# Kernel optimization log

Hardware: AMD Instinct MI355X
Metric: run time of the kernel (lower is better)

The kernel has to match this reference:

```python
import jax, jax.numpy as jnp
import numpy as np

S, B, IN, H, DFF, OUT, L, NHEAD, WINDOW = 2048, 4, 64, 1024, 1024, 64, 3, 4, 4
EPS = 1e-5


def _layer_norm(x, scale, bias):
    m = jnp.mean(x, axis=-1, keepdims=True)
    v = jnp.var(x, axis=-1, keepdims=True)
    return (x - m) * jax.lax.rsqrt(v + EPS) * scale + bias


def setup_inputs() -> dict:
    key = jax.random.key(0)
    ks = jax.random.split(key, 12)
    s = 0.02
    return {
        "src": jax.random.normal(ks[0], (S, B, IN), dtype=jnp.float32),
        "Wenc": jax.random.normal(ks[1], (H, IN), dtype=jnp.float32) * s,
        "benc": jnp.zeros((H,), jnp.float32),
        "Wqkv": jax.random.normal(ks[2], (L, 3 * H, H), dtype=jnp.float32) * s,
        "bqkv": jnp.zeros((L, 3 * H), jnp.float32),
        "Wo": jax.random.normal(ks[3], (L, H, H), dtype=jnp.float32) * s,
        "bo": jnp.zeros((L, H), jnp.float32),
        "W1": jax.random.normal(ks[4], (L, DFF, H), dtype=jnp.float32) * s,
        "b1": jnp.zeros((L, DFF), jnp.float32),
        "W2": jax.random.normal(ks[5], (L, H, DFF), dtype=jnp.float32) * s,
        "b2": jnp.zeros((L, H), jnp.float32),
        "ln1_s": jnp.ones((L, H), jnp.float32),
        "ln1_b": jnp.zeros((L, H), jnp.float32),
        "ln2_s": jnp.ones((L, H), jnp.float32),
        "ln2_b": jnp.zeros((L, H), jnp.float32),
        "Wout": jax.random.normal(ks[6], (OUT, H), dtype=jnp.float32) * s,
        "bout": jnp.zeros((OUT,), jnp.float32),
    }


def _banded_mask(sz):
    # triu(1) masked + lower-band (j < i-4) masked => allowed: i-4 <= j <= i
    i = jnp.arange(sz)[:, None]
    j = jnp.arange(sz)[None, :]
    allowed = (j <= i) & (j >= i - WINDOW)
    return jnp.where(allowed, 0.0, -1e9).astype(jnp.float32)


def reference(src, Wenc, benc, Wqkv, bqkv, Wo, bo, W1, b1, W2, b2,
              ln1_s, ln1_b, ln2_s, ln2_b, Wout, bout):
    dh = H // NHEAD
    mask = _banded_mask(src.shape[0])  # [S, S]
    x = src @ Wenc.T + benc  # [S, B, H]  (NOTE: pos_encoder is never applied in the source)

    def layer(x, p):
        Wqkv_, bqkv_, Wo_, bo_, W1_, b1_, W2_, b2_, s1, g1, s2, g2 = p
        qkv = x @ Wqkv_.T + bqkv_  # [S, B, 3H]
        q, k, v = jnp.split(qkv, 3, axis=-1)
        sS, sB = x.shape[0], x.shape[1]
        q = q.reshape(sS, sB, NHEAD, dh)
        k = k.reshape(sS, sB, NHEAD, dh)
        v = v.reshape(sS, sB, NHEAD, dh)
        scores = jnp.einsum('sbhd,tbhd->bhst', q, k) / jnp.sqrt(jnp.float32(dh))
        scores = scores + mask  # broadcast over [b, h]
        attn = jax.nn.softmax(scores, axis=-1)
        ctx = jnp.einsum('bhst,tbhd->sbhd', attn, v).reshape(sS, sB, H)
        attn_out = ctx @ Wo_.T + bo_
        x = _layer_norm(x + attn_out, s1, g1)  # post-norm (PyTorch default)
        ff = jax.nn.relu(x @ W1_.T + b1_) @ W2_.T + b2_
        x = _layer_norm(x + ff, s2, g2)
        return x, None

    x, _ = jax.lax.scan(layer, x, (Wqkv, bqkv, Wo, bo, W1, b1, W2, b2,
                                   ln1_s, ln1_b, ln2_s, ln2_b))
    return x @ Wout.T + bout  # [S, B, OUT]
```

## Files before the change

### kernel.cpp

```cpp
#include <hip/hip_runtime.h>
#include <hip/hip_bf16.h>

#define S_LEN   2048
#define BATCH   4
#define IN_DIM  64
#define H_DIM   1024
#define DFF_DIM 1024
#define OUT_DIM 64
#define NLAYER  3
#define NHEADS  4
#define DHEAD   256
#define WIN     4
#define ROWS    (S_LEN*BATCH)
#define QKV_LD  (3*H_DIM)


typedef __bf16 bf16x8 __attribute__((ext_vector_type(8)));
typedef float  f32x4  __attribute__((ext_vector_type(4)));

__device__ __forceinline__ float bfbits2f(unsigned int u) {
  union { unsigned int i; float f; } c; c.i = u << 16; return c.f;
}
__device__ __forceinline__ unsigned short f2bfbits(float f) {
  __hip_bfloat16 h = __float2bfloat16(f);
  return __builtin_bit_cast(unsigned short, h);
}

__device__ __forceinline__ void g2l16(const void* g, void* l) {
  __builtin_amdgcn_global_load_lds((__attribute__((address_space(1))) void*)g,
                                   (__attribute__((address_space(3))) void*)l,
                                   16, 0, 0);
}

struct CvtSeg { const float* src; __hip_bfloat16* dst; int n4; };

__global__ __launch_bounds__(256)
void cvt_all_k(CvtSeg s0, CvtSeg s1, CvtSeg s2, CvtSeg s3,
               CvtSeg s4, CvtSeg s5, CvtSeg s6)
{
  int i = blockIdx.x * 256 + threadIdx.x;
  CvtSeg seg;
  if      (i < s0.n4) { seg = s0; }
  else if ((i -= s0.n4) < s1.n4) { seg = s1; }
  else if ((i -= s1.n4) < s2.n4) { seg = s2; }
  else if ((i -= s2.n4) < s3.n4) { seg = s3; }
  else if ((i -= s3.n4) < s4.n4) { seg = s4; }
  else if ((i -= s4.n4) < s5.n4) { seg = s5; }
  else if ((i -= s5.n4) < s6.n4) { seg = s6; }
  else return;
  float4 v = *(const float4*)(seg.src + (size_t)i * 4);
  uint2 o;
  o.x = (unsigned)f2bfbits(v.x) | ((unsigned)f2bfbits(v.y) << 16);
  o.y = (unsigned)f2bfbits(v.z) | ((unsigned)f2bfbits(v.w) << 16);
  *(uint2*)(seg.dst + (size_t)i * 4) = o;
}

template<int RELU, int OUTF32, int ADDRES>
__global__ __launch_bounds__(256, 2)
void gemm_bt(const __hip_bfloat16* __restrict__ A, int lda,
             const __hip_bfloat16* __restrict__ B,
             const float* __restrict__ bias,
             void* __restrict__ Cp, int ldc,
             const __hip_bfloat16* __restrict__ R, int ldr,
             int M, int N, int K)
{
  __shared__ __align__(16) __hip_bfloat16 As[128 * 64];
  __shared__ __align__(16) __hip_bfloat16 Bs[128 * 64];

  const int tid  = threadIdx.x;
  const int lane = tid & 63;
  const int wave = tid >> 6;
  const int quad = lane >> 4;
  const int l16  = lane & 15;

  const int gx  = gridDim.x;
  const int lin = blockIdx.y * gx + blockIdx.x;
  const int gsz = 4 * gx;
  const int mt  = (lin / gsz) * 4 + (lin & 3);
  const int nt  = (lin % gsz) >> 2;
  const int m0 = mt * 128;
  const int n0 = nt * 128;

  const int wr = (wave >> 1) * 64;
  const int wc = (wave & 1) * 64;

  int arow[4], acol[4], brow[4];
#pragma unroll
  for (int s = 0; s < 4; s++) {
    const int p = tid + (s << 8);
    arow[s] = p >> 3;
    acol[s] = ((p & 7) ^ ((p >> 3) & 7)) * 8;
    brow[s] = min(n0 + arow[s], N - 1);
  }

  f32x4 acc[4][4] = {};
  const int nk = K >> 6;

  for (int t = 0; t < nk; ++t) {
    const int k0 = t << 6;
#pragma unroll
    for (int s = 0; s < 4; s++) {
      const int lo = (wave * 64 + (s << 8)) * 8;
      g2l16(A + (size_t)(m0 + arow[s]) * lda + k0 + acol[s], &As[lo]);
      g2l16(B + (size_t)brow[s] * K + k0 + acol[s], &Bs[lo]);
    }
    __syncthreads();

#pragma unroll
    for (int kh = 0; kh < 2; kh++) {
      bf16x8 af[4], bfr[4];
#pragma unroll
      for (int i = 0; i < 4; i++) {
        const int row = wr + i * 16 + l16;
        const int c   = (kh * 4 + quad) ^ (row & 7);
        af[i] = *(const bf16x8*)&As[row * 64 + c * 8];
      }
#pragma unroll
      for (int j = 0; j < 4; j++) {
        const int row = wc + j * 16 + l16;
        const int c   = (kh * 4 + quad) ^ (row & 7);
        bfr[j] = *(const bf16x8*)&Bs[row * 64 + c * 8];
      }
#pragma unroll
      for (int i = 0; i < 4; i++)
#pragma unroll
        for (int j = 0; j < 4; j++)
          acc[i][j] = __builtin_amdgcn_mfma_f32_16x16x32_bf16(af[i], bfr[j], acc[i][j], 0, 0, 0);
    }
    __syncthreads();
  }

#pragma unroll
  for (int j = 0; j < 4; j++) {
    int col = n0 + wc + j * 16 + l16;
    if (col < N) {
      float bv = bias[col];
#pragma unroll
      for (int i = 0; i < 4; i++) {
        int row = m0 + wr + i * 16 + quad * 4;
#pragma unroll
        for (int r = 0; r < 4; r++) {
          float v = acc[i][j][r] + bv;
          if (RELU) v = fmaxf(v, 0.f);
          if (ADDRES) v += __bfloat162float(R[(size_t)(row + r) * ldr + col]);
          if (OUTF32) ((float*)Cp)[(size_t)(row + r) * ldc + col] = v;
          else ((__hip_bfloat16*)Cp)[(size_t)(row + r) * ldc + col] = __float2bfloat16(v);
        }
      }
    }
  }
}

__global__ __launch_bounds__(256)
void attn_k(__hip_bfloat16* __restrict__ qkv)
{
  const int gw   = (blockIdx.x << 2) + (threadIdx.x >> 6);
  const int lane = threadIdx.x & 63;
  const int h = gw & (NHEADS - 1);
  const int b = (gw >> 2) & (BATCH - 1);
  const int s = gw >> 4;
  const size_t hoff = (size_t)h * DHEAD + (lane << 2);

  float q0, q1, q2, q3;
  {
    uint2 t = *(const uint2*)(qkv + (size_t)(s * BATCH + b) * QKV_LD + hoff);
    q0 = bfbits2f(t.x & 0xffff); q1 = bfbits2f(t.x >> 16);
    q2 = bfbits2f(t.y & 0xffff); q3 = bfbits2f(t.y >> 16);
  }

  float sc[WIN + 1];
#pragma unroll
  for (int jj = 0; jj <= WIN; jj++) {
    int j = s - WIN + jj;
    float v = -1e30f;
    if (j >= 0) {
      uint2 t = *(const uint2*)(qkv + (size_t)(j * BATCH + b) * QKV_LD + H_DIM + hoff);
      float p = q0 * bfbits2f(t.x & 0xffff) + q1 * bfbits2f(t.x >> 16)
              + q2 * bfbits2f(t.y & 0xffff) + q3 * bfbits2f(t.y >> 16);
#pragma unroll
      for (int o = 32; o; o >>= 1) p += __shfl_xor(p, o);
      v = p * 0.0625f;
    }
    sc[jj] = v;
  }

  float mx = sc[0];
#pragma unroll
  for (int jj = 1; jj <= WIN; jj++) mx = fmaxf(mx, sc[jj]);
  float p[WIN + 1], den = 0.f;
#pragma unroll
  for (int jj = 0; jj <= WIN; jj++) { p[jj] = __expf(sc[jj] - mx); den += p[jj]; }

  float a0 = 0.f, a1 = 0.f, a2 = 0.f, a3 = 0.f;
#pragma unroll
  for (int jj = 0; jj <= WIN; jj++) {
    int j = s - WIN + jj;
    if (j >= 0) {
      uint2 t = *(const uint2*)(qkv + (size_t)(j * BATCH + b) * QKV_LD + 2 * H_DIM + hoff);
      a0 += p[jj] * bfbits2f(t.x & 0xffff); a1 += p[jj] * bfbits2f(t.x >> 16);
      a2 += p[jj] * bfbits2f(t.y & 0xffff); a3 += p[jj] * bfbits2f(t.y >> 16);
    }
  }
  float rl = 1.f / den;
  uint2 o;
  o.x = (unsigned)f2bfbits(a0 * rl) | ((unsigned)f2bfbits(a1 * rl) << 16);
  o.y = (unsigned)f2bfbits(a2 * rl) | ((unsigned)f2bfbits(a3 * rl) << 16);
  *(uint2*)(qkv + (size_t)(s * BATCH + b) * QKV_LD + hoff) = o;
}

__global__ __launch_bounds__(256)
void ln_k(const __hip_bfloat16* __restrict__ y, int ys,
          const float* __restrict__ g, const float* __restrict__ be,
          __hip_bfloat16* __restrict__ xout)
{
  const int row  = blockIdx.x * 4 + (threadIdx.x >> 6);
  const int lane = threadIdx.x & 63;
  const int e0   = lane * 16;
  const __hip_bfloat16* yp = y + (size_t)row * ys + e0;

  uint2 v[4];
  *(uint4*)&v[0] = *(const uint4*)yp;
  *(uint4*)&v[2] = *(const uint4*)(yp + 8);
  float t[16];
#pragma unroll
  for (int k = 0; k < 4; k++) {
    t[k * 4 + 0] = bfbits2f(v[k].x & 0xffff);
    t[k * 4 + 1] = bfbits2f(v[k].x >> 16);
    t[k * 4 + 2] = bfbits2f(v[k].y & 0xffff);
    t[k * 4 + 3] = bfbits2f(v[k].y >> 16);
  }
  float s = 0.f, ss = 0.f;
#pragma unroll
  for (int k = 0; k < 16; k++) { s += t[k]; ss += t[k] * t[k]; }
#pragma unroll
  for (int o = 32; o; o >>= 1) { s += __shfl_xor(s, o); ss += __shfl_xor(ss, o); }

  const float inv  = 1.f / (float)H_DIM;
  const float mean = s * inv;
  const float var  = ss * inv - mean * mean;
  const float rstd = rsqrtf(var + 1e-5f);

  float4 gv[4], bv[4];
#pragma unroll
  for (int k = 0; k < 4; k++) {
    gv[k] = *(const float4*)(g + e0 + k * 4);
    bv[k] = *(const float4*)(be + e0 + k * 4);
  }
  uint2 ob[4];
#pragma unroll
  for (int k = 0; k < 4; k++) {
    float o0 = (t[k*4+0] - mean) * rstd * gv[k].x + bv[k].x;
    float o1 = (t[k*4+1] - mean) * rstd * gv[k].y + bv[k].y;
    float o2 = (t[k*4+2] - mean) * rstd * gv[k].z + bv[k].z;
    float o3 = (t[k*4+3] - mean) * rstd * gv[k].w + bv[k].w;
    ob[k].x = (unsigned)f2bfbits(o0) | ((unsigned)f2bfbits(o1) << 16);
    ob[k].y = (unsigned)f2bfbits(o2) | ((unsigned)f2bfbits(o3) << 16);
  }
  __hip_bfloat16* xp = xout + (size_t)row * H_DIM + e0;
  *(uint4*)xp       = *(const uint4*)&ob[0];
  *(uint4*)(xp + 8) = *(const uint4*)&ob[2];
}

extern "C" void kernel_launch(void* const* d_in, const int* in_sizes, int n_in,
                              void* d_out, int out_size, void* d_ws, size_t ws_size,
                              hipStream_t stream) {
  const float* src   = (const float*)d_in[0];
  const float* Wenc  = (const float*)d_in[1];
  const float* benc  = (const float*)d_in[2];
  const float* Wqkv  = (const float*)d_in[3];
  const float* bqkv  = (const float*)d_in[4];
  const float* Wo    = (const float*)d_in[5];
  const float* bo    = (const float*)d_in[6];
  const float* W1    = (const float*)d_in[7];
  const float* b1    = (const float*)d_in[8];
  const float* W2    = (const float*)d_in[9];
  const float* b2    = (const float*)d_in[10];
  const float* ln1s  = (const float*)d_in[11];
  const float* ln1b  = (const float*)d_in[12];
  const float* ln2s  = (const float*)d_in[13];
  const float* ln2b  = (const float*)d_in[14];
  const float* Wout  = (const float*)d_in[15];
  const float* bout  = (const float*)d_in[16];

  char* ws = (char*)d_ws;
  __hip_bfloat16* WB   = (__hip_bfloat16*)ws;
  __hip_bfloat16* srcb = WB;
  __hip_bfloat16* wenc = WB + 524288;
  __hip_bfloat16* wqkv = WB + 589824;
  __hip_bfloat16* wo   = WB + 10027008;
  __hip_bfloat16* w1   = WB + 13172736;
  __hip_bfloat16* w2   = WB + 16318464;
  __hip_bfloat16* wout = WB + 19464192;
  __hip_bfloat16* xb  = (__hip_bfloat16*)(ws + (size_t)40 * 1048576);
  __hip_bfloat16* qkv = (__hip_bfloat16*)(ws + (size_t)56 * 1048576);
  __hip_bfloat16* ctxp = qkv;
  __hip_bfloat16* ybuf = qkv + H_DIM;
  __hip_bfloat16* hbuf = qkv + 2 * H_DIM;

  const dim3 blk(256);

  {
    CvtSeg s0{src,  srcb, 524288 / 4};
    CvtSeg s1{Wenc, wenc, 65536 / 4};
    CvtSeg s2{Wqkv, wqkv, 9437184 / 4};
    CvtSeg s3{Wo,   wo,   3145728 / 4};
    CvtSeg s4{W1,   w1,   3145728 / 4};
    CvtSeg s5{W2,   w2,   3145728 / 4};
    CvtSeg s6{Wout, wout, 65536 / 4};
    const int tot4 = (524288 + 65536 + 9437184 + 3 * 3145728 + 65536) / 4;
    cvt_all_k<<<dim3((tot4 + 255) / 256), blk, 0, stream>>>(s0, s1, s2, s3, s4, s5, s6);
  }

  gemm_bt<0, 0, 0><<<dim3(H_DIM / 128, ROWS / 128), blk, 0, stream>>>(
      srcb, IN_DIM, wenc, benc, xb, H_DIM, nullptr, 0, ROWS, H_DIM, IN_DIM);

  for (int l = 0; l < NLAYER; l++) {
    gemm_bt<0, 0, 0><<<dim3(QKV_LD / 128, ROWS / 128), blk, 0, stream>>>(
        xb, H_DIM, wqkv + (size_t)l * QKV_LD * H_DIM, bqkv + l * QKV_LD,
        qkv, QKV_LD, nullptr, 0, ROWS, QKV_LD, H_DIM);
    attn_k<<<dim3(ROWS * NHEADS / 4), blk, 0, stream>>>(qkv);
    gemm_bt<0, 0, 1><<<dim3(H_DIM / 128, ROWS / 128), blk, 0, stream>>>(
        ctxp, QKV_LD, wo + (size_t)l * H_DIM * H_DIM, bo + l * H_DIM,
        ybuf, QKV_LD, xb, H_DIM, ROWS, H_DIM, H_DIM);
    ln_k<<<dim3(ROWS / 4), blk, 0, stream>>>(ybuf, QKV_LD, ln1s + l * H_DIM, ln1b + l * H_DIM, xb);
    gemm_bt<1, 0, 0><<<dim3(DFF_DIM / 128, ROWS / 128), blk, 0, stream>>>(
        xb, H_DIM, w1 + (size_t)l * DFF_DIM * H_DIM, b1 + l * DFF_DIM,
        hbuf, QKV_LD, nullptr, 0, ROWS, DFF_DIM, H_DIM);
    gemm_bt<0, 0, 1><<<dim3(H_DIM / 128, ROWS / 128), blk, 0, stream>>>(
        hbuf, QKV_LD, w2 + (size_t)l * H_DIM * DFF_DIM, b2 + l * H_DIM,
        ybuf, QKV_LD, xb, H_DIM, ROWS, H_DIM, DFF_DIM);
    ln_k<<<dim3(ROWS / 4), blk, 0, stream>>>(ybuf, QKV_LD, ln2s + l * H_DIM, ln2b + l * H_DIM, xb);
  }

  gemm_bt<0, 1, 0><<<dim3(1, ROWS / 128), blk, 0, stream>>>(
      xb, H_DIM, wout, bout, d_out, OUT_DIM, nullptr, 0, ROWS, OUT_DIM, H_DIM);
}
```

Before: 733.4 us.

## Add 256x256 8-wave pipelined GEMM kernel for QKV projection

Adds a new bf16 MFMA GEMM kernel with 512 threads, 256x256 output tiles, a double-buffered and XOR-swizzled LDS layout, and an 8-phase schedule that interleaves global-to-LDS prefetch with MFMA work. It also remaps blocks in groups of four M-tiles for L2 reuse. Only the QKV projection GEMM, the largest one per layer, uses it. The aim is more data reuse per tile and better overlap of memory traffic with compute. The cost is much higher register and LDS pressure, and the kernel assumes K is a multiple of 128 and dimensions divide exactly.

Measured after the change: 746.9 us. Within noise of the previous version (+1.8%).

```diff
diff --git a/kernel.cpp b/kernel.cpp
--- a/kernel.cpp
+++ b/kernel.cpp
@@ -149,6 +149,144 @@
       }
     }
   }
+}
+
+#define G8_STAGE(SLOTPTR, GBASE, LD)                                          \
+  do {                                                                        \
+    const __hip_bfloat16* gb_ = (GBASE);                                      \
+    g2l16(gb_ + (size_t)sr0 * (LD) + sc8x8, (SLOTPTR) + (wave << 9));         \
+    g2l16(gb_ + (size_t)sr1 * (LD) + sc8x8, (SLOTPTR) + 4096 + (wave << 9));  \
+  } while (0)
+
+#define G8_PHASE(BUF, QM, QN, STAGE_STMT, WAIT_STMT)                          \
+  do {                                                                        \
+    bf16x8 af[4][2], bfr[2][2];                                               \
+    const __hip_bfloat16* Asl = &lds[BUF][QM][0];                             \
+    const __hip_bfloat16* Bsl = &lds[BUF][2 + (QN)][0];                       \
+    _Pragma("unroll") for (int im = 0; im < 4; im++) {                        \
+      const int r = wrA + im * 16;                                            \
+      const int sw = r & 7;                                                   \
+      _Pragma("unroll") for (int ks = 0; ks < 2; ks++)                        \
+        af[im][ks] = *(const bf16x8*)&Asl[r * 64 + (((ks * 4 + quad) ^ sw) << 3)]; \
+    }                                                                         \
+    _Pragma("unroll") for (int jn = 0; jn < 2; jn++) {                        \
+      const int r = wrB + jn * 16;                                            \
+      const int sw = r & 7;                                                   \
+      _Pragma("unroll") for (int ks = 0; ks < 2; ks++)                        \
+        bfr[jn][ks] = *(const bf16x8*)&Bsl[r * 64 + (((ks * 4 + quad) ^ sw) << 3)]; \
+    }                                                                         \
+    STAGE_STMT;                                                               \
+    WAIT_STMT;                                                                \
+    __builtin_amdgcn_s_barrier();                                             \
+    asm volatile("s_waitcnt lgkmcnt(0)" ::: "memory");                        \
+    __builtin_amdgcn_sched_barrier(0);                                        \
+    __builtin_amdgcn_s_setprio(1);                                            \
+    _Pragma("unroll") for (int ks = 0; ks < 2; ks++)                          \
+      _Pragma("unroll") for (int im = 0; im < 4; im++)                        \
+        _Pragma("unroll") for (int jn = 0; jn < 2; jn++)                      \
+          acc[(QM) * 4 + im][(QN) * 2 + jn] =                                 \
+              __builtin_amdgcn_mfma_f32_16x16x32_bf16(                        \
+                  af[im][ks], bfr[jn][ks],                                    \
+                  acc[(QM) * 4 + im][(QN) * 2 + jn], 0, 0, 0);                \
+    __builtin_amdgcn_s_setprio(0);                                            \
+    __builtin_amdgcn_s_barrier();                                             \
+  } while (0)
+
+template<int RELU, int ADDRES>
+__global__ __launch_bounds__(512, 2)
+void gemm8_bt(const __hip_bfloat16* __restrict__ A, int lda,
+              const __hip_bfloat16* __restrict__ B,
+              const float* __restrict__ bias,
+              __hip_bfloat16* __restrict__ C, int ldc,
+              const __hip_bfloat16* __restrict__ Rr, int ldr,
+              int N, int K)
+{
+  __shared__ __align__(16) __hip_bfloat16 lds[2][4][128 * 64];
+
+  const int tid  = threadIdx.x;
+  const int lane = tid & 63;
+  const int wave = tid >> 6;
+  const int quad = lane >> 4;
+  const int l16  = lane & 15;
+  const int wm   = wave >> 2;
+  const int wn   = wave & 3;
+  const int wrA  = wm * 64 + l16;
+  const int wrB  = wn * 32 + l16;
+
+  const int sr0   = tid >> 3;
+  const int sr1   = sr0 + 64;
+  const int sc8x8 = (((tid & 7) ^ (sr0 & 7)) << 3);
+
+  const int gx  = gridDim.x;
+  const int lin = blockIdx.y * gx + blockIdx.x;
+  const int gsz = 4 * gx;
+  const int mt  = (lin / gsz) * 4 + (lin & 3);
+  const int nt  = (lin % gsz) >> 2;
+  const int m0 = mt * 256;
+  const int n0 = nt * 256;
+
+  const __hip_bfloat16* Ab = A + (size_t)m0 * lda;
+  const __hip_bfloat16* Bb = B + (size_t)n0 * K;
+
+  f32x4 acc[8][4] = {};
+  const int NI = K >> 7;
+
+  G8_STAGE(&lds[0][0][0], Ab, lda);
+  G8_STAGE(&lds[0][2][0], Bb, K);
+  G8_STAGE(&lds[0][1][0], Ab + (size_t)128 * lda, lda);
+  G8_STAGE(&lds[0][3][0], Bb + (size_t)128 * K, K);
+  G8_STAGE(&lds[1][0][0], Ab + 64, lda);
+  G8_STAGE(&lds[1][2][0], Bb + 64, K);
+  asm volatile("s_waitcnt vmcnt(4)" ::: "memory");
+  __builtin_amdgcn_s_barrier();
+
+  for (int i = 0; i < NI; ++i) {
+    const int k1 = (2 * i + 1) << 6;
+    const int k2 = k1 + 64;
+    const int k3 = k1 + 128;
+    const bool pf = (i + 1 < NI);
+
+    G8_PHASE(0, 0, 0,
+             G8_STAGE(&lds[1][1][0], Ab + (size_t)128 * lda + k1, lda), );
+    G8_PHASE(0, 0, 1,
+             G8_STAGE(&lds[1][3][0], Bb + (size_t)128 * K + k1, K), );
+    G8_PHASE(0, 1, 0,
+             if (pf) G8_STAGE(&lds[0][0][0], Ab + k2, lda), );
+    G8_PHASE(0, 1, 1,
+             if (pf) G8_STAGE(&lds[0][2][0], Bb + k2, K),
+             if (pf) { asm volatile("s_waitcnt vmcnt(4)" ::: "memory"); }
+             else    { asm volatile("s_waitcnt vmcnt(0)" ::: "memory"); });
+    G8_PHASE(1, 0, 0,
+             if (pf) G8_STAGE(&lds[0][1][0], Ab + (size_t)128 * lda + k2, lda), );
+    G8_PHASE(1, 0, 1,
+             if (pf) G8_STAGE(&lds[0][3][0], Bb + (size_t)128 * K + k2, K), );
+    G8_PHASE(1, 1, 0,
+             if (pf) G8_STAGE(&lds[1][0][0], Ab + k3, lda), );
+    G8_PHASE(1, 1, 1,
+             if (pf) G8_STAGE(&lds[1][2][0], Bb + k3, K),
+             asm volatile("s_waitcnt vmcnt(4)" ::: "memory"));
+  }
+
+#pragma unroll
+  for (int qm = 0; qm < 2; qm++)
+#pragma unroll
+    for (int im = 0; im < 4; im++)
+#pragma unroll
+      for (int qn = 0; qn < 2; qn++)
+#pragma unroll
+        for (int jn = 0; jn < 2; jn++) {
+          const int row0 = m0 + qm * 128 + wm * 64 + im * 16 + quad * 4;
+          const int col  = n0 + qn * 128 + wn * 32 + jn * 16 + l16;
+          const float bv = bias[col];
+          const f32x4 a  = acc[qm * 4 + im][qn * 2 + jn];
+#pragma unroll
+          for (int r = 0; r < 4; r++) {
+            float v = a[r] + bv;
+            if (RELU) v = fmaxf(v, 0.f);
+            if (ADDRES) v += __bfloat162float(Rr[(size_t)(row0 + r) * ldr + col]);
+            C[(size_t)(row0 + r) * ldc + col] = __float2bfloat16(v);
+          }
+        }
 }
 
 __global__ __launch_bounds__(256)
@@ -315,9 +453,9 @@
       srcb, IN_DIM, wenc, benc, xb, H_DIM, nullptr, 0, ROWS, H_DIM, IN_DIM);
 
   for (int l = 0; l < NLAYER; l++) {
-    gemm_bt<0, 0, 0><<<dim3(QKV_LD / 128, ROWS / 128), blk, 0, stream>>>(
+    gemm8_bt<0, 0><<<dim3(QKV_LD / 256, ROWS / 256), dim3(512), 0, stream>>>(
         xb, H_DIM, wqkv + (size_t)l * QKV_LD * H_DIM, bqkv + l * QKV_LD,
-        qkv, QKV_LD, nullptr, 0, ROWS, QKV_LD, H_DIM);
+        qkv, QKV_LD, nullptr, 0, QKV_LD, H_DIM);
     attn_k<<<dim3(ROWS * NHEADS / 4), blk, 0, stream>>>(qkv);
     gemm_bt<0, 0, 1><<<dim3(H_DIM / 128, ROWS / 128), blk, 0, stream>>>(
         ctxp, QKV_LD, wo + (size_t)l * H_DIM * H_DIM, bo + l * H_DIM,
```

## Add triple-buffered 128x256 GEMM kernel with async LDS loads for layer GEMMs

Applied to the files above, without the earlier changes.

Introduces a new 512-thread GEMM kernel that uses 128x256 tiles, a three-stage LDS ring buffer filled by direct global-to-LDS loads, XOR-swizzled LDS layout, grouped tile rasterization, and split-phase prefetch interleaved with MFMA issue under raised wave priority. All four per-layer GEMMs switch to it. The aim is to hide global memory latency behind matrix work and raise per-block reuse over the older 128x128 kernel. In exchange it uses much more LDS per block, limiting occupancy to one block per CU, and it relies on the dimensions being exact multiples of the tile sizes.

Result: faster. 697.7 us (-4.9%).

```diff
diff --git a/kernel.cpp b/kernel.cpp
--- a/kernel.cpp
+++ b/kernel.cpp
@@ -146,6 +146,134 @@
           if (OUTF32) ((float*)Cp)[(size_t)(row + r) * ldc + col] = v;
           else ((__hip_bfloat16*)Cp)[(size_t)(row + r) * ldc + col] = __float2bfloat16(v);
         }
+      }
+    }
+  }
+}
+
+#define R3_SA(BUF, KO)                                                        \
+  do {                                                                        \
+    __hip_bfloat16* d_ = &lds[BUF][0];                                        \
+    _Pragma("unroll") for (int s_ = 0; s_ < 2; s_++)                          \
+      g2l16(Ab + (size_t)arow[s_] * lda + (KO) + acol[s_],                    \
+            d_ + (((wave << 6) + (s_ << 9)) << 3));                           \
+  } while (0)
+#define R3_SB0(BUF, KO)                                                       \
+  do {                                                                        \
+    __hip_bfloat16* d_ = &lds[BUF][8192];                                     \
+    _Pragma("unroll") for (int s_ = 0; s_ < 2; s_++)                          \
+      g2l16(Bb + (size_t)arow[s_] * K + (KO) + acol[s_],                      \
+            d_ + (((wave << 6) + (s_ << 9)) << 3));                           \
+  } while (0)
+#define R3_SB1(BUF, KO)                                                       \
+  do {                                                                        \
+    __hip_bfloat16* d_ = &lds[BUF][8192];                                     \
+    _Pragma("unroll") for (int s_ = 2; s_ < 4; s_++)                          \
+      g2l16(Bb + (size_t)arow[s_] * K + (KO) + acol[s_],                      \
+            d_ + (((wave << 6) + (s_ << 9)) << 3));                           \
+  } while (0)
+
+#define R3_PH(BUF, KS, STAGE_STMT, WAIT_STMT)                                 \
+  do {                                                                        \
+    bf16x8 af[4], bq[4];                                                      \
+    const __hip_bfloat16* As_ = &lds[BUF][0];                                 \
+    const __hip_bfloat16* Bs_ = &lds[BUF][8192];                              \
+    _Pragma("unroll") for (int im = 0; im < 4; im++) {                        \
+      const int r_ = wm * 64 + im * 16 + l16;                                 \
+      af[im] = *(const bf16x8*)&As_[r_ * 64 + ((((KS)*4 + quad) ^ (r_ & 7)) << 3)]; \
+    }                                                                         \
+    _Pragma("unroll") for (int jn = 0; jn < 4; jn++) {                        \
+      const int r_ = wn * 64 + jn * 16 + l16;                                 \
+      bq[jn] = *(const bf16x8*)&Bs_[r_ * 64 + ((((KS)*4 + quad) ^ (r_ & 7)) << 3)]; \
+    }                                                                         \
+    STAGE_STMT;                                                               \
+    WAIT_STMT;                                                                \
+    __builtin_amdgcn_s_barrier();                                             \
+    asm volatile("s_waitcnt lgkmcnt(0)" ::: "memory");                        \
+    __builtin_amdgcn_sched_barrier(0);                                        \
+    __builtin_amdgcn_s_setprio(1);                                            \
+    _Pragma("unroll") for (int im = 0; im < 4; im++)                          \
+      _Pragma("unroll") for (int jn = 0; jn < 4; jn++)                        \
+        acc[im][jn] = __builtin_amdgcn_mfma_f32_16x16x32_bf16(                \
+            af[im], bq[jn], acc[im][jn], 0, 0, 0);                            \
+    __builtin_amdgcn_s_setprio(0);                                            \
+    __builtin_amdgcn_s_barrier();                                             \
+  } while (0)
+
+template<int RELU, int ADDRES>
+__global__ __launch_bounds__(512, 1)
+void gemm3r_bt(const __hip_bfloat16* __restrict__ A, int lda,
+               const __hip_bfloat16* __restrict__ B,
+               const float* __restrict__ bias,
+               __hip_bfloat16* __restrict__ C, int ldc,
+               const __hip_bfloat16* __restrict__ Rr, int ldr,
+               int K)
+{
+  __shared__ __align__(16) __hip_bfloat16 lds[3][24576];
+
+  const int tid  = threadIdx.x;
+  const int lane = tid & 63;
+  const int wave = tid >> 6;
+  const int quad = lane >> 4;
+  const int l16  = lane & 15;
+  const int wm   = wave >> 2;
+  const int wn   = wave & 3;
+
+  const int gx  = gridDim.x;
+  const int lin = blockIdx.y * gx + blockIdx.x;
+  const int gsz = 4 * gx;
+  const int mt  = (lin / gsz) * 4 + (lin & 3);
+  const int nt  = (lin % gsz) >> 2;
+  const int m0 = mt * 128;
+  const int n0 = nt * 256;
+
+  const __hip_bfloat16* Ab = A + (size_t)m0 * lda;
+  const __hip_bfloat16* Bb = B + (size_t)n0 * K;
+
+  int arow[4], acol[4];
+#pragma unroll
+  for (int s = 0; s < 4; s++) {
+    const int p = tid + (s << 9);
+    arow[s] = p >> 3;
+    acol[s] = ((p & 7) ^ (arow[s] & 7)) << 3;
+  }
+
+  f32x4 acc[4][4] = {};
+  const int NK = K >> 6;
+
+  R3_SA(0, 0);  R3_SB0(0, 0);  R3_SB1(0, 0);
+  R3_SA(1, 64); R3_SB0(1, 64); R3_SB1(1, 64);
+  asm volatile("s_waitcnt vmcnt(6)" ::: "memory");
+  __builtin_amdgcn_s_barrier();
+
+  for (int t = 0; t < NK; ++t) {
+    const int r  = t % 3;
+    const int rn = (t + 2) % 3;
+    const int k2 = (t + 2) << 6;
+    const bool pf = (t + 2) < NK;
+
+    R3_PH(r, 0,
+          if (pf) { R3_SA(rn, k2); R3_SB0(rn, k2); }, );
+    R3_PH(r, 1,
+          if (pf) { R3_SB1(rn, k2); },
+          if (pf) { asm volatile("s_waitcnt vmcnt(6)" ::: "memory"); }
+          else    { asm volatile("s_waitcnt vmcnt(0)" ::: "memory"); });
+  }
+
+#pragma unroll
+  for (int jn = 0; jn < 4; jn++) {
+    const int col = n0 + wn * 64 + jn * 16 + l16;
+    const float bv = bias[col];
+#pragma unroll
+    for (int im = 0; im < 4; im++) {
+      const int row0 = m0 + wm * 64 + im * 16 + quad * 4;
+      const f32x4 a = acc[im][jn];
+#pragma unroll
+      for (int rr = 0; rr < 4; rr++) {
+        float v = a[rr] + bv;
+        if (RELU) v = fmaxf(v, 0.f);
+        if (ADDRES) v += __bfloat162float(Rr[(size_t)(row0 + rr) * ldr + col]);
+        C[(size_t)(row0 + rr) * ldc + col] = __float2bfloat16(v);
       }
     }
   }
@@ -298,6 +426,7 @@
   __hip_bfloat16* hbuf = qkv + 2 * H_DIM;
 
   const dim3 blk(256);
+  const dim3 blk512(512);
 
   {
     CvtSeg s0{src,  srcb, 524288 / 4};
@@ -315,20 +444,20 @@
       srcb, IN_DIM, wenc, benc, xb, H_DIM, nullptr, 0, ROWS, H_DIM, IN_DIM);
 
   for (int l = 0; l < NLAYER; l++) {
-    gemm_bt<0, 0, 0><<<dim3(QKV_LD / 128, ROWS / 128), blk, 0, stream>>>(
+    gemm3r_bt<0, 0><<<dim3(QKV_LD / 256, ROWS / 128), blk512, 0, stream>>>(
         xb, H_DIM, wqkv + (size_t)l * QKV_LD * H_DIM, bqkv + l * QKV_LD,
-        qkv, QKV_LD, nullptr, 0, ROWS, QKV_LD, H_DIM);
+        qkv, QKV_LD, nullptr, 0, H_DIM);
     attn_k<<<dim3(ROWS * NHEADS / 4), blk, 0, stream>>>(qkv);
-    gemm_bt<0, 0, 1><<<dim3(H_DIM / 128, ROWS / 128), blk, 0, stream>>>(
+    gemm3r_bt<0, 1><<<dim3(H_DIM / 256, ROWS / 128), blk512, 0, stream>>>(
         ctxp, QKV_LD, wo + (size_t)l * H_DIM * H_DIM, bo + l * H_DIM,
-        ybuf, QKV_LD, xb, H_DIM, ROWS, H_DIM, H_DIM);
+        ybuf, QKV_LD, xb, H_DIM, H_DIM);
     ln_k<<<dim3(ROWS / 4), blk, 0, stream>>>(ybuf, QKV_LD, ln1s + l * H_DIM, ln1b + l * H_DIM, xb);
-    gemm_bt<1, 0, 0><<<dim3(DFF_DIM / 128, ROWS / 128), blk, 0, stream>>>(
+    gemm3r_bt<1, 0><<<dim3(DFF_DIM / 256, ROWS / 128), blk512, 0, stream>>>(
         xb, H_DIM, w1 + (size_t)l * DFF_DIM * H_DIM, b1 + l * DFF_DIM,
-        hbuf, QKV_LD, nullptr, 0, ROWS, DFF_DIM, H_DIM);
-    gemm_bt<0, 0, 1><<<dim3(H_DIM / 128, ROWS / 128), blk, 0, stream>>>(
+        hbuf, QKV_LD, nullptr, 0, H_DIM);
+    gemm3r_bt<0, 1><<<dim3(H_DIM / 256, ROWS / 128), blk512, 0, stream>>>(
         hbuf, QKV_LD, w2 + (size_t)l * H_DIM * DFF_DIM, b2 + l * H_DIM,
-        ybuf, QKV_LD, xb, H_DIM, ROWS, H_DIM, DFF_DIM);
+        ybuf, QKV_LD, xb, H_DIM, DFF_DIM);
     ln_k<<<dim3(ROWS / 4), blk, 0, stream>>>(ybuf, QKV_LD, ln2s + l * H_DIM, ln2b + l * H_DIM, xb);
   }
 
```
